# Kernel optimization log

Measured on AMD Instinct MI355X. Metric: run time of the kernel, lower is better.

## Reference

```python
import jax, jax.numpy as jnp
import numpy as np


def setup_inputs() -> dict:
    key = jax.random.key(0)
    k1, k2, k3 = jax.random.split(key, 3)
    num_paths, horizon, d_obs = 1024, 64, 64
    d_input = int(d_obs + d_obs * (d_obs + 1) / 2 + 1)  # 2145
    observations = jax.random.normal(k1, (num_paths, horizon, d_obs), dtype=jnp.float32)
    weights = jax.random.normal(k2, (horizon, d_input), dtype=jnp.float32)
    biases = jax.random.normal(k3, (horizon,), dtype=jnp.float32)
    return {"observations": observations, "weights": weights, "biases": biases}


def reference(observations, weights, biases):
    # observations: [N, H, D]; weights: [H, D + D*(D+1)/2 + 1]; biases: [H]
    d_obs = observations.shape[-1]
    iu, ju = jnp.triu_indices(d_obs)  # upper-triangular (i <= j) pairs, matching the torch loop order
    quad = observations[..., iu] * observations[..., ju]      # [N, H, D*(D+1)/2]
    feats = jnp.concatenate([observations, quad], axis=-1)    # [N, H, d_input-1]
    # The torch code leaves the last feature column as zero, so weights[:, -1]
    # contributes nothing; slice it off instead of materializing a zero column.
    values = jnp.einsum("nhd,hd->nh", feats, weights[:, :-1]) + biases
    return values
```

## Files before the change

kernel.cpp:

```cpp
#include <hip/hip_runtime.h>


#define DOBS 64
#define NH   64
#define WROW 2145
#define NQUAD 2080
#define LSTR 72

typedef unsigned short u16;
typedef __attribute__((ext_vector_type(8))) short short8;
typedef __attribute__((ext_vector_type(4))) short short4v;
typedef __attribute__((ext_vector_type(4))) float floatx4;

__device__ __forceinline__ u16 f2bf(float f) {
    unsigned u = __float_as_uint(f);
    return (u16)((u + 0x7FFF + ((u >> 16) & 1)) >> 16);
}
__device__ __forceinline__ float bf2f(u16 b) {
    return __uint_as_float(((unsigned)b) << 16);
}
__device__ __forceinline__ int tri_start(int i) {
    return (i * (129 - i)) >> 1;
}

__global__ __launch_bounds__(256) void qvf_main(
    const float* __restrict__ obs, const float* __restrict__ weights,
    const float* __restrict__ biases, float* __restrict__ out, int N)
{
    __shared__ u16 O16[DOBS * LSTR];
    __shared__ u16 W16[DOBS * LSTR];
    __shared__ float LW[DOBS];

    const int h    = blockIdx.x & (NH - 1);
    const int tidx = blockIdx.x >> 6;
    const int lane = threadIdx.x & 63;
    const int wv   = threadIdx.x >> 6;
    const int n0   = tidx * 64;

    const float* __restrict__ wsrc = weights + h * WROW;

    float wq[8];
#pragma unroll
    for (int p = 0; p < 8; ++p)
        wq[p] = wsrc[DOBS + p * 256 + threadIdx.x];
    float wq8 = 0.f;
    if (threadIdx.x < NQUAD - 2048)
        wq8 = wsrc[DOBS + 2048 + threadIdx.x];

    if (threadIdx.x < DOBS) LW[threadIdx.x] = wsrc[threadIdx.x];

    {
        const short8 z = (short8)0;
        *(short8*)&W16[threadIdx.x * 8]         = z;
        *(short8*)&W16[(256 + threadIdx.x) * 8] = z;
        if (threadIdx.x < 64) *(short8*)&W16[(512 + threadIdx.x) * 8] = z;
    }

    {
        const float* __restrict__ src = obs + ((size_t)n0 * NH + h) * DOBS;
#pragma unroll
        for (int p = 0; p < 4; ++p) {
            const int g  = p * 256 + threadIdx.x;
            const int r  = g >> 4;
            const int c4 = g & 15;
            const floatx4 v = *(const floatx4*)(src + (size_t)r * (NH * DOBS) + c4 * 4);
            short4v sv;
            sv[0] = (short)f2bf(v.x); sv[1] = (short)f2bf(v.y);
            sv[2] = (short)f2bf(v.z); sv[3] = (short)f2bf(v.w);
            *(short4v*)&O16[r * LSTR + c4 * 4] = sv;
        }
    }
    __syncthreads();

#pragma unroll
    for (int p = 0; p < 9; ++p) {
        const int q = p * 256 + threadIdx.x;
        if (p == 8 && q >= NQUAD) break;
        const float v = (p < 8) ? wq[p] : wq8;
        const int   t = 16641 - 8 * q;
        int i = (int)((129.0f - __builtin_sqrtf((float)t)) * 0.5f);
        i = (i < 0) ? 0 : ((i > 63) ? 63 : i);
        if (q < tri_start(i)) --i;
        if (q >= tri_start(i + 1)) ++i;
        const int j = i + (q - tri_start(i));
        W16[i * LSTR + j] = f2bf(v);
    }
    __syncthreads();

    const int col = lane & 15;
    const int qq  = lane >> 4;
    floatx4 acc[4];
#pragma unroll
    for (int ct = 0; ct < 4; ++ct) {
        const float wl = LW[ct * 16 + col];
        acc[ct][0] = wl; acc[ct][1] = wl; acc[ct][2] = wl; acc[ct][3] = wl;
    }

    const int mrow = wv * 16 + col;
#pragma unroll
    for (int ks = 0; ks < 2; ++ks) {
        const short8 a = *(const short8*)&O16[mrow * LSTR + ks * 32 + qq * 8];
#pragma unroll
        for (int ct = 0; ct < 4; ++ct) {
            const int i = ct * 16 + col;
            const short8 b = *(const short8*)&W16[i * LSTR + ks * 32 + qq * 8];
            acc[ct] = __builtin_amdgcn_mfma_f32_16x16x32_bf16(a, b, acc[ct], 0, 0, 0);
        }
    }

    float P[4] = {0.f, 0.f, 0.f, 0.f};
#pragma unroll
    for (int ct = 0; ct < 4; ++ct) {
#pragma unroll
        for (int r = 0; r < 4; ++r) {
            const int row = wv * 16 + qq * 4 + r;
            const u16 ov = O16[row * LSTR + ct * 16 + col];
            P[r] = fmaf(acc[ct][r], bf2f(ov), P[r]);
        }
    }
#pragma unroll
    for (int msk = 1; msk < 16; msk <<= 1) {
#pragma unroll
        for (int r = 0; r < 4; ++r) P[r] += __shfl_xor(P[r], msk, 64);
    }
    if (col == 0) {
        const float b = biases[h];
#pragma unroll
        for (int r = 0; r < 4; ++r) {
            const int row = wv * 16 + qq * 4 + r;
            out[(size_t)(n0 + row) * NH + h] = P[r] + b;
        }
    }
}

extern "C" void kernel_launch(void* const* d_in, const int* in_sizes, int n_in,
                              void* d_out, int out_size, void* d_ws, size_t ws_size,
                              hipStream_t stream) {
    const float* obs     = (const float*)d_in[0];
    const float* weights = (const float*)d_in[1];
    const float* biases  = (const float*)d_in[2];
    float* out           = (float*)d_out;

    const int N = in_sizes[0] / (NH * DOBS);
    qvf_main<<<dim3((N / 64) * NH), dim3(256), 0, stream>>>(obs, weights, biases, out, N);
}
```

Baseline: 68.40 us.

## Precompute dense bf16 weight matrices once in a prep kernel

Adds a prep kernel that scatters each horizon's triangular quadratic weights into a padded dense bf16 matrix, plus the linear weights, and stores them in workspace. The main kernel then copies this dense layout straight into shared memory instead of redoing the sqrt-based index decode and conversion in every one of the 16 blocks per horizon. It also issues the observation loads before the weight loads so their latencies overlap. The cost is an extra kernel launch and a global round trip through the workspace.

Result: slower. 70.08 us (+2.5%).

```diff
diff --git a/kernel.cpp b/kernel.cpp
--- a/kernel.cpp
+++ b/kernel.cpp
@@ -23,20 +23,12 @@
     return (i * (129 - i)) >> 1;
 }
 
-__global__ __launch_bounds__(256) void qvf_main(
-    const float* __restrict__ obs, const float* __restrict__ weights,
-    const float* __restrict__ biases, float* __restrict__ out, int N)
+__global__ __launch_bounds__(256) void qvf_prep(
+    const float* __restrict__ weights, u16* __restrict__ wdense,
+    float* __restrict__ lwdense)
 {
-    __shared__ u16 O16[DOBS * LSTR];
     __shared__ u16 W16[DOBS * LSTR];
-    __shared__ float LW[DOBS];
-
-    const int h    = blockIdx.x & (NH - 1);
-    const int tidx = blockIdx.x >> 6;
-    const int lane = threadIdx.x & 63;
-    const int wv   = threadIdx.x >> 6;
-    const int n0   = tidx * 64;
-
+    const int h = blockIdx.x;
     const float* __restrict__ wsrc = weights + h * WROW;
 
     float wq[8];
@@ -47,28 +39,14 @@
     if (threadIdx.x < NQUAD - 2048)
         wq8 = wsrc[DOBS + 2048 + threadIdx.x];
 
-    if (threadIdx.x < DOBS) LW[threadIdx.x] = wsrc[threadIdx.x];
+    if (threadIdx.x < DOBS)
+        lwdense[h * DOBS + threadIdx.x] = wsrc[threadIdx.x];
 
     {
         const short8 z = (short8)0;
         *(short8*)&W16[threadIdx.x * 8]         = z;
         *(short8*)&W16[(256 + threadIdx.x) * 8] = z;
         if (threadIdx.x < 64) *(short8*)&W16[(512 + threadIdx.x) * 8] = z;
-    }
-
-    {
-        const float* __restrict__ src = obs + ((size_t)n0 * NH + h) * DOBS;
-#pragma unroll
-        for (int p = 0; p < 4; ++p) {
-            const int g  = p * 256 + threadIdx.x;
-            const int r  = g >> 4;
-            const int c4 = g & 15;
-            const floatx4 v = *(const floatx4*)(src + (size_t)r * (NH * DOBS) + c4 * 4);
-            short4v sv;
-            sv[0] = (short)f2bf(v.x); sv[1] = (short)f2bf(v.y);
-            sv[2] = (short)f2bf(v.z); sv[3] = (short)f2bf(v.w);
-            *(short4v*)&O16[r * LSTR + c4 * 4] = sv;
-        }
     }
     __syncthreads();
 
@@ -84,6 +62,59 @@
         if (q >= tri_start(i + 1)) ++i;
         const int j = i + (q - tri_start(i));
         W16[i * LSTR + j] = f2bf(v);
+    }
+    __syncthreads();
+
+    u16* __restrict__ dst = wdense + h * (DOBS * LSTR);
+    *(short8*)&dst[threadIdx.x * 8]         = *(const short8*)&W16[threadIdx.x * 8];
+    *(short8*)&dst[(256 + threadIdx.x) * 8] = *(const short8*)&W16[(256 + threadIdx.x) * 8];
+    if (threadIdx.x < 64)
+        *(short8*)&dst[(512 + threadIdx.x) * 8] = *(const short8*)&W16[(512 + threadIdx.x) * 8];
+}
+
+__global__ __launch_bounds__(256) void qvf_main(
+    const float* __restrict__ obs, const u16* __restrict__ wdense,
+    const float* __restrict__ lwdense, const float* __restrict__ biases,
+    float* __restrict__ out)
+{
+    __shared__ u16 O16[DOBS * LSTR];
+    __shared__ u16 W16[DOBS * LSTR];
+    __shared__ float LW[DOBS];
+
+    const int h    = blockIdx.x & (NH - 1);
+    const int tidx = blockIdx.x >> 6;
+    const int lane = threadIdx.x & 63;
+    const int wv   = threadIdx.x >> 6;
+    const int n0   = tidx * 64;
+
+    const float* __restrict__ src = obs + ((size_t)n0 * NH + h) * DOBS;
+    floatx4 ov[4];
+#pragma unroll
+    for (int p = 0; p < 4; ++p) {
+        const int g  = p * 256 + threadIdx.x;
+        const int r  = g >> 4;
+        const int c4 = g & 15;
+        ov[p] = *(const floatx4*)(src + (size_t)r * (NH * DOBS) + c4 * 4);
+    }
+    const u16* __restrict__ wsrc = wdense + h * (DOBS * LSTR);
+    const short8 w0 = *(const short8*)(wsrc + threadIdx.x * 8);
+    const short8 w1 = *(const short8*)(wsrc + (256 + threadIdx.x) * 8);
+    short8 w2 = (short8)0;
+    if (threadIdx.x < 64) w2 = *(const short8*)(wsrc + (512 + threadIdx.x) * 8);
+    if (threadIdx.x < DOBS) LW[threadIdx.x] = lwdense[h * DOBS + threadIdx.x];
+
+    *(short8*)&W16[threadIdx.x * 8]         = w0;
+    *(short8*)&W16[(256 + threadIdx.x) * 8] = w1;
+    if (threadIdx.x < 64) *(short8*)&W16[(512 + threadIdx.x) * 8] = w2;
+#pragma unroll
+    for (int p = 0; p < 4; ++p) {
+        const int g  = p * 256 + threadIdx.x;
+        const int r  = g >> 4;
+        const int c4 = g & 15;
+        short4v sv;
+        sv[0] = (short)f2bf(ov[p].x); sv[1] = (short)f2bf(ov[p].y);
+        sv[2] = (short)f2bf(ov[p].z); sv[3] = (short)f2bf(ov[p].w);
+        *(short4v*)&O16[r * LSTR + c4 * 4] = sv;
     }
     __syncthreads();
 
@@ -114,8 +145,8 @@
 #pragma unroll
         for (int r = 0; r < 4; ++r) {
             const int row = wv * 16 + qq * 4 + r;
-            const u16 ov = O16[row * LSTR + ct * 16 + col];
-            P[r] = fmaf(acc[ct][r], bf2f(ov), P[r]);
+            const u16 ovl = O16[row * LSTR + ct * 16 + col];
+            P[r] = fmaf(acc[ct][r], bf2f(ovl), P[r]);
         }
     }
 #pragma unroll
@@ -141,6 +172,11 @@
     const float* biases  = (const float*)d_in[2];
     float* out           = (float*)d_out;
 
+    u16*   wdense  = (u16*)d_ws;
+    float* lwdense = (float*)((char*)d_ws + (size_t)NH * DOBS * LSTR * sizeof(u16));
+
     const int N = in_sizes[0] / (NH * DOBS);
-    qvf_main<<<dim3((N / 64) * NH), dim3(256), 0, stream>>>(obs, weights, biases, out, N);
+
+    qvf_prep<<<dim3(NH), dim3(256), 0, stream>>>(weights, wdense, lwdense);
+    qvf_main<<<dim3((N / 64) * NH), dim3(256), 0, stream>>>(obs, wdense, lwdense, biases, out);
 }
```
